# Performance work log

Hardware: AMD Instinct MI355X
Metric: run time of the kernel (lower is better)

## Reference

```python
import jax, jax.numpy as jnp
import numpy as np
import math

B, S, P, G = 8, 512, 64, 64
E, GE = 768, 32          # sub_embed_dim, gene_embed_dim
HD = E // 2              # sub_head_dim = 384
L = P * G
LAMBDA_INIT = 0.8 - 0.6 * math.exp(-0.3 * 0)  # depth=0 -> 0.2
SCALING = HD ** -0.5


def setup_inputs() -> dict:
    key0 = jax.random.key(0)
    ks = jax.random.split(key0, 12)
    init = 0.02
    return {
        "query": jax.random.normal(ks[0], (B, S, E), jnp.float32),
        "key": jax.random.normal(ks[1], (B, P, G, GE), jnp.float32),
        "query_mask": jax.random.bernoulli(ks[2], 0.9, (B, S)),
        "key_mask": jax.random.bernoulli(ks[3], 0.9, (B, P, G)),
        # weights stored [in, out] so y = x @ W (equiv to torch Linear no-bias)
        "Wq": jax.random.normal(ks[4], (E, E), jnp.float32) * init,
        "Wkv": jax.random.normal(ks[5], (GE, 2 * E), jnp.float32) * init,
        "Wout": jax.random.normal(ks[6], (E, E), jnp.float32) * init,
        "lambda_q1": jax.random.normal(ks[7], (HD,), jnp.float32) * 0.1,
        "lambda_k1": jax.random.normal(ks[8], (HD,), jnp.float32) * 0.1,
        "lambda_q2": jax.random.normal(ks[9], (HD,), jnp.float32) * 0.1,
        "lambda_k2": jax.random.normal(ks[10], (HD,), jnp.float32) * 0.1,
        "ln_weight": jnp.ones((E,), jnp.float32),  # RMSNorm affine weight (2*HD = E)
    }


def reference(query, key, query_mask, key_mask, Wq, Wkv, Wout,
              lambda_q1, lambda_k1, lambda_q2, lambda_k2, ln_weight):
    # Projections
    Q = query @ Wq                                   # [B,S,E]
    KV = key.reshape(B, L, GE) @ Wkv                 # [B,L,2E]
    K = KV[..., :E]                                  # [B,L,E]
    V = KV[..., E:]                                  # [B,L,E] (= 2*HD)

    # Split into 2 heads of dim HD
    Qh = Q.reshape(B, S, 2, HD).transpose(0, 2, 1, 3) * SCALING   # [B,2,S,HD]
    Kh = K.reshape(B, L, 2, HD).transpose(0, 2, 1, 3)             # [B,2,L,HD]

    # Combined mask [B,S,L]
    mask = query_mask[:, :, None] & key_mask.reshape(B, L)[:, None, :]

    # Dual attention scores + stable softmax (eps=1e-8 on denominator)
    scores = jnp.einsum('bhsd,bhld->bhsl', Qh, Kh)                # [B,2,S,L]
    scores = jnp.where(mask[:, None], scores, -1e20)
    m = jnp.max(scores, axis=-1, keepdims=True)
    p = jnp.exp(scores - m)
    attn = p / (jnp.sum(p, axis=-1, keepdims=True) + 1e-8)

    # Differential combination
    lam = (jnp.exp(jnp.sum(lambda_q1 * lambda_k1))
           - jnp.exp(jnp.sum(lambda_q2 * lambda_k2)) + LAMBDA_INIT)
    diff = attn[:, 0] - lam * attn[:, 1]                          # [B,S,L]
    diff = diff - jnp.min(diff, axis=-1, keepdims=True) + 1e-20
    diff = jnp.where(mask, diff, 0.0)

    # Value contraction: [B,S,L] @ [B,L,E] -> [B,S,E]
    attn_out = jnp.einsum('bsl,ble->bse', diff, V)

    # RMSNorm (eps=1e-5, affine) then scale by (1 - lambda_init)
    ms = jnp.mean(attn_out * attn_out, axis=-1, keepdims=True)
    attn_out = attn_out * jax.lax.rsqrt(ms + 1e-5) * ln_weight
    attn_out = attn_out * (1.0 - LAMBDA_INIT)

    out = attn_out @ Wout                                         # [B,S,E]
    return out, diff.reshape(B, S, P, G)
```

## Files before the change

kernel.cpp:

```cpp
#include <hip/hip_runtime.h>
#include <math.h>

#define LAM_INIT 0.2f
#define ONE_MINUS_LAM 0.8f
#define SCALING_F 0.05103103630798288f

__device__ inline float waveMax(float v) {
#pragma unroll
    for (int o = 32; o > 0; o >>= 1) v = fmaxf(v, __shfl_xor(v, o));
    return v;
}
__device__ inline float waveMin(float v) {
#pragma unroll
    for (int o = 32; o > 0; o >>= 1) v = fminf(v, __shfl_xor(v, o));
    return v;
}
__device__ inline float waveSum(float v) {
#pragma unroll
    for (int o = 32; o > 0; o >>= 1) v += __shfl_xor(v, o);
    return v;
}

__global__ __launch_bounds__(256) void k01_prep(
    const float* __restrict__ key, const float* __restrict__ Wq,
    const float* __restrict__ Wkv, const float* __restrict__ Wout,
    const float* __restrict__ lq1, const float* __restrict__ lk1,
    const float* __restrict__ lq2, const float* __restrict__ lk2,
    const float* __restrict__ ln,
    float* __restrict__ keyT, float* __restrict__ Wcomb,
    float* __restrict__ Wvo, float* __restrict__ lam)
{
    int blk = blockIdx.x;
    int tid = threadIdx.x;
    if (blk < 128) {
        int b  = blk >> 4;
        int l0 = (blk & 15) << 8;
        __shared__ float tile[256 * 33];
        const float* kp = key + ((size_t)b * 4096 + l0) * 32;
#pragma unroll
        for (int q = 0; q < 32; ++q) {
            int idx = tid + (q << 8);
            int r = idx >> 5, g = idx & 31;
            tile[r * 33 + g] = kp[idx];
        }
        __syncthreads();
        float* op = keyT + (size_t)b * 32 * 4096 + l0;
#pragma unroll
        for (int q = 0; q < 32; ++q) {
            int idx = tid + (q << 8);
            int g = idx >> 8, ll = idx & 255;
            op[(size_t)g * 4096 + ll] = tile[ll * 33 + g];
        }
    } else if (blk < 512) {
        int bb = blk - 128;
        int kc = bb & 1;
        int ob = bb >> 1;
        int idx = ob * 256 + tid;
        int e  = idx >> 6;
        int hg = idx & 63;
        int h = hg >> 5, g = hg & 31;
        const float4* wqr = (const float4*)(Wq  + (size_t)e * 768 + h * 384 + kc * 192);
        const float4* wkr = (const float4*)(Wkv + (size_t)g * 1536 + h * 384 + kc * 192);
        float s0 = 0.f, s1 = 0.f;
#pragma unroll 4
        for (int d = 0; d < 48; d += 2) {
            float4 a0 = wqr[d],   b0 = wkr[d];
            float4 a1 = wqr[d+1], b1 = wkr[d+1];
            s0 += a0.x*b0.x + a0.y*b0.y + a0.z*b0.z + a0.w*b0.w;
            s1 += a1.x*b1.x + a1.y*b1.y + a1.z*b1.z + a1.w*b1.w;
        }
        atomicAdd(&Wcomb[idx], (s0 + s1) * SCALING_F);
    } else if (blk < 1280) {
        int bb = blk - 512;
        int kc = bb / 96;
        int ob = bb - kc * 96;
        int idx = ob * 256 + tid;
        int g = idx / 768;
        int e = idx - g * 768;
        const float* wvr = Wkv + (size_t)g * 1536 + 768;
        int c0 = kc * 96;
        float s0 = 0.f, s1 = 0.f;
#pragma unroll 4
        for (int c = c0; c < c0 + 96; c += 2) {
            s0 += wvr[c]   * ln[c]   * Wout[(size_t)c * 768 + e];
            s1 += wvr[c+1] * ln[c+1] * Wout[(size_t)(c+1) * 768 + e];
        }
        atomicAdd(&Wvo[idx], s0 + s1);
    } else {
        float s1 = 0.f, s2 = 0.f;
        for (int d = tid; d < 384; d += 256) {
            s1 += lq1[d] * lk1[d];
            s2 += lq2[d] * lk2[d];
        }
        s1 = waveSum(s1);
        s2 = waveSum(s2);
        __shared__ float r1[4], r2[4];
        int wid = tid >> 6, lane = tid & 63;
        if (lane == 0) { r1[wid] = s1; r2[wid] = s2; }
        __syncthreads();
        if (tid == 0) {
            float a  = r1[0] + r1[1] + r1[2] + r1[3];
            float b2 = r2[0] + r2[1] + r2[2] + r2[3];
            lam[0] = expf(a) - expf(b2) + LAM_INIT;
        }
    }
}

__global__ __launch_bounds__(256) void k2_qt(
    const float* __restrict__ query, const float* __restrict__ Wcomb,
    float* __restrict__ Qt)
{
    int m0 = blockIdx.x * 32;
    int tid = threadIdx.x;
    int tx = tid & 15;
    int ty = tid >> 4;
    __shared__ __align__(16) float As[32 * 36];
    __shared__ __align__(16) float Bs[32 * 64];
    float acc[2][4] = {{0.f,0.f,0.f,0.f},{0.f,0.f,0.f,0.f}};

    for (int k0 = 0; k0 < 768; k0 += 32) {
        __syncthreads();
#pragma unroll
        for (int q = 0; q < 4; ++q) {
            int idx = tid + q * 256;
            int r = idx >> 5, c = idx & 31;
            As[r * 36 + c] = query[(size_t)(m0 + r) * 768 + k0 + c];
        }
#pragma unroll
        for (int q = 0; q < 8; ++q) {
            int idx = tid + q * 256;
            int r = idx >> 6, c = idx & 63;
            Bs[r * 64 + c] = Wcomb[(size_t)(k0 + r) * 64 + c];
        }
        __syncthreads();
#pragma unroll
        for (int kk = 0; kk < 32; kk += 4) {
            float4 a0 = *(const float4*)&As[(ty * 2 + 0) * 36 + kk];
            float4 a1 = *(const float4*)&As[(ty * 2 + 1) * 36 + kk];
            float4 b0 = *(const float4*)&Bs[(kk + 0) * 64 + tx * 4];
            float4 b1 = *(const float4*)&Bs[(kk + 1) * 64 + tx * 4];
            float4 b2 = *(const float4*)&Bs[(kk + 2) * 64 + tx * 4];
            float4 b3 = *(const float4*)&Bs[(kk + 3) * 64 + tx * 4];
            acc[0][0] += a0.x*b0.x + a0.y*b1.x + a0.z*b2.x + a0.w*b3.x;
            acc[0][1] += a0.x*b0.y + a0.y*b1.y + a0.z*b2.y + a0.w*b3.y;
            acc[0][2] += a0.x*b0.z + a0.y*b1.z + a0.z*b2.z + a0.w*b3.z;
            acc[0][3] += a0.x*b0.w + a0.y*b1.w + a0.z*b2.w + a0.w*b3.w;
            acc[1][0] += a1.x*b0.x + a1.y*b1.x + a1.z*b2.x + a1.w*b3.x;
            acc[1][1] += a1.x*b0.y + a1.y*b1.y + a1.z*b2.y + a1.w*b3.y;
            acc[1][2] += a1.x*b0.z + a1.y*b1.z + a1.z*b2.z + a1.w*b3.z;
            acc[1][3] += a1.x*b0.w + a1.y*b1.w + a1.z*b2.w + a1.w*b3.w;
        }
    }
#pragma unroll
    for (int rr = 0; rr < 2; ++rr) {
        float4 o; o.x = acc[rr][0]; o.y = acc[rr][1]; o.z = acc[rr][2]; o.w = acc[rr][3];
        *(float4*)&Qt[(size_t)(m0 + ty * 2 + rr) * 64 + tx * 4] = o;
    }
}

__global__ __launch_bounds__(512, 4) void k3_attn(
    const float* __restrict__ Qt, const float* __restrict__ keyT,
    const int* __restrict__ qmask, const int* __restrict__ kmask,
    const float* __restrict__ lamp, float* __restrict__ diffO)
{
    int blk = blockIdx.x;
    int b  = blk >> 7;
    int s0 = (blk & 127) * 4;
    int tid = threadIdx.x;
    int lane = tid & 63, wid = tid >> 6;

    __shared__ __align__(16) float qt_t[32 * 8];
    __shared__ float red[64];

    if (tid < 256) {
        int ts = tid >> 6, c2 = tid & 63;
        int h = c2 >> 5, g = c2 & 31;
        qt_t[g * 8 + (ts << 1) + h] = Qt[(size_t)(b * 512 + s0 + ts) * 64 + c2];
    }
    int qm[4];
#pragma unroll
    for (int ts = 0; ts < 4; ++ts) qm[ts] = qmask[b * 512 + s0 + ts];
    float lam = lamp[0];

    unsigned kmb = 0;
#pragma unroll
    for (int c = 0; c < 2; ++c) {
        int4 km = *(const int4*)(kmask + b * 4096 + c * 2048 + tid * 4);
        if (km.x) kmb |= 1u << (c * 4 + 0);
        if (km.y) kmb |= 1u << (c * 4 + 1);
        if (km.z) kmb |= 1u << (c * 4 + 2);
        if (km.w) kmb |= 1u << (c * 4 + 3);
    }
    __syncthreads();

    float p[2][4][8];
#pragma unroll
    for (int h = 0; h < 2; ++h)
#pragma unroll
        for (int ts = 0; ts < 4; ++ts)
#pragma unroll
            for (int i = 0; i < 8; ++i) p[h][ts][i] = 0.f;

    const float* kt = keyT + (size_t)b * 131072 + tid * 4;
    for (int g = 0; g < 32; ++g) {
        float qv[8];
        *(float4*)&qv[0] = *(const float4*)&qt_t[g * 8];
        *(float4*)&qv[4] = *(const float4*)&qt_t[g * 8 + 4];
        const float* kg = kt + (size_t)g * 4096;
#pragma unroll
        for (int c = 0; c < 2; ++c) {
            float4 kv = *(const float4*)(kg + c * 2048);
#pragma unroll
            for (int ts = 0; ts < 4; ++ts)
#pragma unroll
                for (int h = 0; h < 2; ++h) {
                    float q = qv[ts * 2 + h];
                    p[h][ts][c*4+0] += q * kv.x;
                    p[h][ts][c*4+1] += q * kv.y;
                    p[h][ts][c*4+2] += q * kv.z;
                    p[h][ts][c*4+3] += q * kv.w;
                }
        }
    }

#pragma unroll
    for (int h = 0; h < 2; ++h)
#pragma unroll
        for (int ts = 0; ts < 4; ++ts)
#pragma unroll
            for (int i = 0; i < 8; ++i) {
                bool ok = qm[ts] && ((kmb >> i) & 1u);
                p[h][ts][i] = ok ? p[h][ts][i] : -1e20f;
            }

    float mrow[2][4];
#pragma unroll
    for (int h = 0; h < 2; ++h)
#pragma unroll
        for (int ts = 0; ts < 4; ++ts) {
            float v = -3.4e38f;
#pragma unroll
            for (int i = 0; i < 8; ++i) v = fmaxf(v, p[h][ts][i]);
            v = waveMax(v);
            if (lane == 0) red[(h * 4 + ts) * 8 + wid] = v;
        }
    __syncthreads();
#pragma unroll
    for (int h = 0; h < 2; ++h)
#pragma unroll
        for (int ts = 0; ts < 4; ++ts) {
            int r = (h * 4 + ts) * 8;
            float v = red[r];
#pragma unroll
            for (int w = 1; w < 8; ++w) v = fmaxf(v, red[r + w]);
            mrow[h][ts] = v;
        }
    __syncthreads();

    float inv[2][4];
#pragma unroll
    for (int h = 0; h < 2; ++h)
#pragma unroll
        for (int ts = 0; ts < 4; ++ts) {
            float s = 0.f;
#pragma unroll
            for (int i = 0; i < 8; ++i) {
                float e2 = __expf(p[h][ts][i] - mrow[h][ts]);
                p[h][ts][i] = e2;
                s += e2;
            }
            s = waveSum(s);
            if (lane == 0) red[(h * 4 + ts) * 8 + wid] = s;
        }
    __syncthreads();
#pragma unroll
    for (int h = 0; h < 2; ++h)
#pragma unroll
        for (int ts = 0; ts < 4; ++ts) {
            int r = (h * 4 + ts) * 8;
            float s = red[r];
#pragma unroll
            for (int w = 1; w < 8; ++w) s += red[r + w];
            inv[h][ts] = 1.0f / (s + 1e-8f);
        }
    __syncthreads();

    float mn[4];
#pragma unroll
    for (int ts = 0; ts < 4; ++ts) {
        float v = 3.4e38f;
#pragma unroll
        for (int i = 0; i < 8; ++i) {
            float d = p[0][ts][i] * inv[0][ts] - lam * (p[1][ts][i] * inv[1][ts]);
            p[0][ts][i] = d;
            v = fminf(v, d);
        }
        v = waveMin(v);
        if (lane == 0) red[ts * 8 + wid] = v;
    }
    __syncthreads();
#pragma unroll
    for (int ts = 0; ts < 4; ++ts) {
        int r = ts * 8;
        float v = red[r];
#pragma unroll
        for (int w = 1; w < 8; ++w) v = fminf(v, red[r + w]);
        mn[ts] = v;
    }

#pragma unroll
    for (int ts = 0; ts < 4; ++ts) {
        size_t base = (size_t)(b * 512 + s0 + ts) * 4096 + tid * 4;
#pragma unroll
        for (int c = 0; c < 2; ++c) {
            float4 o;
            float v0 = p[0][ts][c*4+0] - mn[ts] + 1e-20f;
            float v1 = p[0][ts][c*4+1] - mn[ts] + 1e-20f;
            float v2 = p[0][ts][c*4+2] - mn[ts] + 1e-20f;
            float v3 = p[0][ts][c*4+3] - mn[ts] + 1e-20f;
            o.x = (qm[ts] && ((kmb >> (c*4+0)) & 1u)) ? v0 : 0.f;
            o.y = (qm[ts] && ((kmb >> (c*4+1)) & 1u)) ? v1 : 0.f;
            o.z = (qm[ts] && ((kmb >> (c*4+2)) & 1u)) ? v2 : 0.f;
            o.w = (qm[ts] && ((kmb >> (c*4+3)) & 1u)) ? v3 : 0.f;
            *(float4*)(diffO + base + c * 2048) = o;
        }
    }
}

__global__ __launch_bounds__(256) void k4_T(
    const float* __restrict__ diff, const float* __restrict__ key,
    float* __restrict__ T)
{
    int blk = blockIdx.x;
    int rt = blk & 31, kc = blk >> 5;
    int row0 = rt << 7;
    int b = row0 >> 9;
    int l0 = kc << 8;
    int tid = threadIdx.x;
    int tx = tid & 7;
    int ty = tid >> 3;
    int g0 = tx * 4;

    __shared__ __align__(16) float Ks[256][32];
#pragma unroll
    for (int q = 0; q < 32; ++q) {
        int idx = tid + (q << 8);
        int r = idx >> 5, g = idx & 31;
        Ks[r][g] = key[((size_t)(b * 4096 + l0 + r)) * 32 + g];
    }
    __syncthreads();

    float acc[4][4];
#pragma unroll
    for (int r = 0; r < 4; ++r)
#pragma unroll
        for (int c2 = 0; c2 < 4; ++c2) acc[r][c2] = 0.f;

    for (int j4 = 0; j4 < 64; ++j4) {
        int l = l0 + j4 * 4;
        float4 dv[4];
#pragma unroll
        for (int r = 0; r < 4; ++r)
            dv[r] = *(const float4*)(diff + (size_t)(row0 + ty * 4 + r) * 4096 + l);
#pragma unroll
        for (int jj = 0; jj < 4; ++jj) {
            float4 kq = *(const float4*)&Ks[j4 * 4 + jj][g0];
#pragma unroll
            for (int r = 0; r < 4; ++r) {
                float d = (jj == 0) ? dv[r].x : (jj == 1) ? dv[r].y : (jj == 2) ? dv[r].z : dv[r].w;
                acc[r][0] += d * kq.x;
                acc[r][1] += d * kq.y;
                acc[r][2] += d * kq.z;
                acc[r][3] += d * kq.w;
            }
        }
    }
#pragma unroll
    for (int r = 0; r < 4; ++r)
#pragma unroll
        for (int c2 = 0; c2 < 4; ++c2)
            atomicAdd(&T[(size_t)(row0 + ty * 4 + r) * 32 + g0 + c2], acc[r][c2]);
}

__global__ __launch_bounds__(256) void k5_out(
    const float* __restrict__ T, const float* __restrict__ Wkv,
    const float* __restrict__ Wvo, float* __restrict__ out)
{
    int row0 = blockIdx.x * 8;
    int tid = threadIdx.x;
    int wid = tid >> 6, lane = tid & 63;
    __shared__ __align__(16) float Ts[8][32];
    __shared__ float red[8][4];
    __shared__ float rs_s[8];

    {
        int r = tid >> 5, g = tid & 31;
        Ts[r][g] = T[(size_t)(row0 + r) * 32 + g];
    }
    __syncthreads();

    float ssq[8];
#pragma unroll
    for (int r = 0; r < 8; ++r) ssq[r] = 0.f;

#pragma unroll
    for (int ec = 0; ec < 3; ++ec) {
        int e = tid + ec * 256;
        float wv[32];
#pragma unroll
        for (int g = 0; g < 32; ++g) wv[g] = Wkv[(size_t)g * 1536 + 768 + e];
#pragma unroll
        for (int r = 0; r < 8; ++r) {
            float a = 0.f;
#pragma unroll
            for (int g = 0; g < 32; ++g) a += Ts[r][g] * wv[g];
            ssq[r] += a * a;
        }
    }
#pragma unroll
    for (int r = 0; r < 8; ++r) {
        float v = waveSum(ssq[r]);
        if (lane == 0) red[r][wid] = v;
    }
    __syncthreads();
    if (tid < 8) {
        float s = red[tid][0] + red[tid][1] + red[tid][2] + red[tid][3];
        float ms = s * (1.0f / 768.0f);
        rs_s[tid] = rsqrtf(ms + 1e-5f) * ONE_MINUS_LAM;
    }
    __syncthreads();

#pragma unroll
    for (int ec = 0; ec < 3; ++ec) {
        int e = tid + ec * 256;
        float wo[32];
#pragma unroll
        for (int g = 0; g < 32; ++g) wo[g] = Wvo[(size_t)g * 768 + e];
#pragma unroll
        for (int r = 0; r < 8; ++r) {
            float o = 0.f;
#pragma unroll
            for (int g = 0; g < 32; ++g) o += Ts[r][g] * wo[g];
            out[(size_t)(row0 + r) * 768 + e] = o * rs_s[r];
        }
    }
}

extern "C" void kernel_launch(void* const* d_in, const int* in_sizes, int n_in,
                              void* d_out, int out_size, void* d_ws, size_t ws_size,
                              hipStream_t stream) {
    (void)in_sizes; (void)n_in; (void)out_size; (void)ws_size;
    const float* query = (const float*)d_in[0];
    const float* key   = (const float*)d_in[1];
    const int*   qmask = (const int*)d_in[2];
    const int*   kmask = (const int*)d_in[3];
    const float* Wq    = (const float*)d_in[4];
    const float* Wkv   = (const float*)d_in[5];
    const float* Wout  = (const float*)d_in[6];
    const float* lq1   = (const float*)d_in[7];
    const float* lk1   = (const float*)d_in[8];
    const float* lq2   = (const float*)d_in[9];
    const float* lk2   = (const float*)d_in[10];
    const float* ln    = (const float*)d_in[11];

    float* out  = (float*)d_out;
    float* diff = out + 3145728;

    float* ws    = (float*)d_ws;
    float* Wcomb = ws;
    float* Wvo   = ws + 49152;
    float* T     = ws + 73728;
    float* lam   = ws + 204800;
    float* Qt    = ws + 204864;
    float* keyT  = ws + 467008;

    hipMemsetAsync(ws, 0, 204800 * sizeof(float), stream);
    k01_prep<<<1281, 256, 0, stream>>>(key, Wq, Wkv, Wout, lq1, lk1, lq2, lk2, ln,
                                       keyT, Wcomb, Wvo, lam);
    k2_qt<<<128, 256, 0, stream>>>(query, Wcomb, Qt);
    k3_attn<<<1024, 512, 0, stream>>>(Qt, keyT, qmask, kmask, lam, diff);
    k4_T<<<512, 256, 0, stream>>>(diff, key, T);
    k5_out<<<512, 256, 0, stream>>>(T, Wkv, Wvo, out);
}
```

Before: 279.2 us.

## Replace float atomics with partial buffers and deterministic reductions across kernels

The Wvo and T accumulations now write per-chunk partial sums to workspace buffers instead of using atomicAdd. The partials are reduced later: Wvo in extra blocks of the Qt kernel, T inside k5 while loading. k4 now processes two K-chunks per block to halve the number of partials, and the Qt GEMM is reworked so each 16-row tile stages query rows in LDS and reads Wcomb directly. This removes atomic contention and most of the memset, at the cost of extra workspace traffic and fewer k4 blocks.

New measurement: 269.3 us. 1.04x faster.

```diff
diff --git a/kernel.cpp b/kernel.cpp
--- a/kernel.cpp
+++ b/kernel.cpp
@@ -28,7 +28,7 @@
     const float* __restrict__ lq2, const float* __restrict__ lk2,
     const float* __restrict__ ln,
     float* __restrict__ keyT, float* __restrict__ Wcomb,
-    float* __restrict__ Wvo, float* __restrict__ lam)
+    float* __restrict__ Wvp, float* __restrict__ lam)
 {
     int blk = blockIdx.x;
     int tid = threadIdx.x;
@@ -85,7 +85,7 @@
             s0 += wvr[c]   * ln[c]   * Wout[(size_t)c * 768 + e];
             s1 += wvr[c+1] * ln[c+1] * Wout[(size_t)(c+1) * 768 + e];
         }
-        atomicAdd(&Wvo[idx], s0 + s1);
+        Wvp[kc * 24576 + idx] = s0 + s1;
     } else {
         float s1 = 0.f, s2 = 0.f;
         for (int d = tid; d < 384; d += 256) {
@@ -108,54 +108,44 @@
 
 __global__ __launch_bounds__(256) void k2_qt(
     const float* __restrict__ query, const float* __restrict__ Wcomb,
+    const float* __restrict__ Wvp, float* __restrict__ Wvo,
     float* __restrict__ Qt)
 {
-    int m0 = blockIdx.x * 32;
+    int blk = blockIdx.x;
     int tid = threadIdx.x;
-    int tx = tid & 15;
-    int ty = tid >> 4;
-    __shared__ __align__(16) float As[32 * 36];
-    __shared__ __align__(16) float Bs[32 * 64];
-    float acc[2][4] = {{0.f,0.f,0.f,0.f},{0.f,0.f,0.f,0.f}};
-
-    for (int k0 = 0; k0 < 768; k0 += 32) {
-        __syncthreads();
-#pragma unroll
-        for (int q = 0; q < 4; ++q) {
-            int idx = tid + q * 256;
-            int r = idx >> 5, c = idx & 31;
-            As[r * 36 + c] = query[(size_t)(m0 + r) * 768 + k0 + c];
-        }
-#pragma unroll
-        for (int q = 0; q < 8; ++q) {
-            int idx = tid + q * 256;
-            int r = idx >> 6, c = idx & 63;
-            Bs[r * 64 + c] = Wcomb[(size_t)(k0 + r) * 64 + c];
-        }
-        __syncthreads();
-#pragma unroll
-        for (int kk = 0; kk < 32; kk += 4) {
-            float4 a0 = *(const float4*)&As[(ty * 2 + 0) * 36 + kk];
-            float4 a1 = *(const float4*)&As[(ty * 2 + 1) * 36 + kk];
-            float4 b0 = *(const float4*)&Bs[(kk + 0) * 64 + tx * 4];
-            float4 b1 = *(const float4*)&Bs[(kk + 1) * 64 + tx * 4];
-            float4 b2 = *(const float4*)&Bs[(kk + 2) * 64 + tx * 4];
-            float4 b3 = *(const float4*)&Bs[(kk + 3) * 64 + tx * 4];
-            acc[0][0] += a0.x*b0.x + a0.y*b1.x + a0.z*b2.x + a0.w*b3.x;
-            acc[0][1] += a0.x*b0.y + a0.y*b1.y + a0.z*b2.y + a0.w*b3.y;
-            acc[0][2] += a0.x*b0.z + a0.y*b1.z + a0.z*b2.z + a0.w*b3.z;
-            acc[0][3] += a0.x*b0.w + a0.y*b1.w + a0.z*b2.w + a0.w*b3.w;
-            acc[1][0] += a1.x*b0.x + a1.y*b1.x + a1.z*b2.x + a1.w*b3.x;
-            acc[1][1] += a1.x*b0.y + a1.y*b1.y + a1.z*b2.y + a1.w*b3.y;
-            acc[1][2] += a1.x*b0.z + a1.y*b1.z + a1.z*b2.z + a1.w*b3.z;
-            acc[1][3] += a1.x*b0.w + a1.y*b1.w + a1.z*b2.w + a1.w*b3.w;
-        }
-    }
-#pragma unroll
-    for (int rr = 0; rr < 2; ++rr) {
-        float4 o; o.x = acc[rr][0]; o.y = acc[rr][1]; o.z = acc[rr][2]; o.w = acc[rr][3];
-        *(float4*)&Qt[(size_t)(m0 + ty * 2 + rr) * 64 + tx * 4] = o;
-    }
+    if (blk >= 256) {
+        int idx = (blk - 256) * 256 + tid;
+        float s = 0.f;
+#pragma unroll
+        for (int kc = 0; kc < 8; ++kc) s += Wvp[kc * 24576 + idx];
+        Wvo[idx] = s;
+        return;
+    }
+    int m0 = blk * 16;
+    __shared__ __align__(16) float Aq[16 * 772];
+#pragma unroll
+    for (int q = 0; q < 12; ++q) {
+        int f = tid + q * 256;
+        int r = f / 192, c4 = f - r * 192;
+        float4 v = *(const float4*)&query[(size_t)(m0 + r) * 768 + c4 * 4];
+        *(float4*)&Aq[r * 772 + c4 * 4] = v;
+    }
+    __syncthreads();
+
+    int n0 = (tid & 15) * 4;
+    int ml = tid >> 4;
+    const float* arow = &Aq[ml * 772];
+    float ax = 0.f, ay = 0.f, az = 0.f, aw = 0.f;
+    for (int k = 0; k < 768; k += 8) {
+#pragma unroll
+        for (int j = 0; j < 8; ++j) {
+            float a = arow[k + j];
+            float4 w = *(const float4*)&Wcomb[(size_t)(k + j) * 64 + n0];
+            ax += a * w.x; ay += a * w.y; az += a * w.z; aw += a * w.w;
+        }
+    }
+    float4 o; o.x = ax; o.y = ay; o.z = az; o.w = aw;
+    *(float4*)&Qt[(size_t)(m0 + ml) * 64 + n0] = o;
 }
 
 __global__ __launch_bounds__(512, 4) void k3_attn(
@@ -329,26 +319,19 @@
 
 __global__ __launch_bounds__(256) void k4_T(
     const float* __restrict__ diff, const float* __restrict__ key,
-    float* __restrict__ T)
+    float* __restrict__ P)
 {
     int blk = blockIdx.x;
     int rt = blk & 31, kc = blk >> 5;
     int row0 = rt << 7;
     int b = row0 >> 9;
-    int l0 = kc << 8;
+    int l0 = kc << 9;
     int tid = threadIdx.x;
     int tx = tid & 7;
     int ty = tid >> 3;
     int g0 = tx * 4;
 
     __shared__ __align__(16) float Ks[256][32];
-#pragma unroll
-    for (int q = 0; q < 32; ++q) {
-        int idx = tid + (q << 8);
-        int r = idx >> 5, g = idx & 31;
-        Ks[r][g] = key[((size_t)(b * 4096 + l0 + r)) * 32 + g];
-    }
-    __syncthreads();
 
     float acc[4][4];
 #pragma unroll
@@ -356,34 +339,46 @@
 #pragma unroll
         for (int c2 = 0; c2 < 4; ++c2) acc[r][c2] = 0.f;
 
-    for (int j4 = 0; j4 < 64; ++j4) {
-        int l = l0 + j4 * 4;
-        float4 dv[4];
-#pragma unroll
-        for (int r = 0; r < 4; ++r)
-            dv[r] = *(const float4*)(diff + (size_t)(row0 + ty * 4 + r) * 4096 + l);
-#pragma unroll
-        for (int jj = 0; jj < 4; ++jj) {
-            float4 kq = *(const float4*)&Ks[j4 * 4 + jj][g0];
-#pragma unroll
-            for (int r = 0; r < 4; ++r) {
-                float d = (jj == 0) ? dv[r].x : (jj == 1) ? dv[r].y : (jj == 2) ? dv[r].z : dv[r].w;
-                acc[r][0] += d * kq.x;
-                acc[r][1] += d * kq.y;
-                acc[r][2] += d * kq.z;
-                acc[r][3] += d * kq.w;
+    for (int ph = 0; ph < 2; ++ph) {
+        int lp = l0 + ph * 256;
+        __syncthreads();
+#pragma unroll
+        for (int q = 0; q < 32; ++q) {
+            int idx = tid + (q << 8);
+            int r = idx >> 5, g = idx & 31;
+            Ks[r][g] = key[((size_t)(b * 4096 + lp + r)) * 32 + g];
+        }
+        __syncthreads();
+
+        for (int j4 = 0; j4 < 64; ++j4) {
+            int l = lp + j4 * 4;
+            float4 dv[4];
+#pragma unroll
+            for (int r = 0; r < 4; ++r)
+                dv[r] = *(const float4*)(diff + (size_t)(row0 + ty * 4 + r) * 4096 + l);
+#pragma unroll
+            for (int jj = 0; jj < 4; ++jj) {
+                float4 kq = *(const float4*)&Ks[j4 * 4 + jj][g0];
+#pragma unroll
+                for (int r = 0; r < 4; ++r) {
+                    float d = (jj == 0) ? dv[r].x : (jj == 1) ? dv[r].y : (jj == 2) ? dv[r].z : dv[r].w;
+                    acc[r][0] += d * kq.x;
+                    acc[r][1] += d * kq.y;
+                    acc[r][2] += d * kq.z;
+                    acc[r][3] += d * kq.w;
+                }
             }
         }
     }
 #pragma unroll
-    for (int r = 0; r < 4; ++r)
-#pragma unroll
-        for (int c2 = 0; c2 < 4; ++c2)
-            atomicAdd(&T[(size_t)(row0 + ty * 4 + r) * 32 + g0 + c2], acc[r][c2]);
+    for (int r = 0; r < 4; ++r) {
+        float4 o; o.x = acc[r][0]; o.y = acc[r][1]; o.z = acc[r][2]; o.w = acc[r][3];
+        *(float4*)&P[(size_t)kc * 131072 + (size_t)(row0 + ty * 4 + r) * 32 + g0] = o;
+    }
 }
 
 __global__ __launch_bounds__(256) void k5_out(
-    const float* __restrict__ T, const float* __restrict__ Wkv,
+    const float* __restrict__ P, const float* __restrict__ Wkv,
     const float* __restrict__ Wvo, float* __restrict__ out)
 {
     int row0 = blockIdx.x * 8;
@@ -395,7 +390,11 @@
 
     {
         int r = tid >> 5, g = tid & 31;
-        Ts[r][g] = T[(size_t)(row0 + r) * 32 + g];
+        float s = 0.f;
+#pragma unroll
+        for (int kc = 0; kc < 8; ++kc)
+            s += P[(size_t)kc * 131072 + (size_t)(row0 + r) * 32 + g];
+        Ts[r][g] = s;
     }
     __syncthreads();
 
@@ -469,16 +468,17 @@
     float* ws    = (float*)d_ws;
     float* Wcomb = ws;
     float* Wvo   = ws + 49152;
-    float* T     = ws + 73728;
-    float* lam   = ws + 204800;
-    float* Qt    = ws + 204864;
-    float* keyT  = ws + 467008;
-
-    hipMemsetAsync(ws, 0, 204800 * sizeof(float), stream);
+    float* Wvp   = ws + 73728;
+    float* lam   = ws + 270336;
+    float* Qt    = ws + 270400;
+    float* keyT  = ws + 532544;
+    float* P     = ws + 1581120;
+
+    hipMemsetAsync(Wcomb, 0, 49152 * sizeof(float), stream);
     k01_prep<<<1281, 256, 0, stream>>>(key, Wq, Wkv, Wout, lq1, lk1, lq2, lk2, ln,
-                                       keyT, Wcomb, Wvo, lam);
-    k2_qt<<<128, 256, 0, stream>>>(query, Wcomb, Qt);
+                                       keyT, Wcomb, Wvp, lam);
+    k2_qt<<<352, 256, 0, stream>>>(query, Wcomb, Wvp, Wvo, Qt);
     k3_attn<<<1024, 512, 0, stream>>>(Qt, keyT, qmask, kmask, lam, diff);
-    k4_T<<<512, 256, 0, stream>>>(diff, key, T);
-    k5_out<<<512, 256, 0, stream>>>(T, Wkv, Wvo, out);
-}
+    k4_T<<<256, 256, 0, stream>>>(diff, key, P);
+    k5_out<<<512, 256, 0, stream>>>(P, Wkv, Wvo, out);
+}
```
